# Kernel optimization log

Measured on AMD Instinct MI355X. Metric: run time of the kernel, lower is better.

The kernel has to match this reference:

```python
import jax, jax.numpy as jnp
import numpy as np
import math

FRAME_SIZE = 576
GAMMA = 0.5
NUM_HEADS = 32


def rotate_half(x):
    x1, x2 = jnp.split(x, 2, axis=-1)
    return jnp.concatenate([-x2, x1], axis=-1)


def apply_rope(x, freqs):
    return x * jnp.cos(freqs) + rotate_half(x) * jnp.sin(freqs)


def rope_freqs(length, dim):
    theta = 10000.0 ** (-jnp.arange(0, dim, 2, dtype=jnp.float32) / dim)
    f = jnp.arange(length, dtype=jnp.float32)[:, None] * theta[None, :]  # [L, dim/2]
    return jnp.concatenate([f, f], axis=-1)  # [L, dim]


def setup_inputs() -> dict:
    key = jax.random.key(0)
    ks = jax.random.split(key, 9)
    B, T, C = 2, 2048, 2048
    s = 0.02  # init scale for projection weights
    return {
        "hidden_states": jax.random.normal(ks[0], (B, T, C), jnp.float32),
        "Wq": jax.random.normal(ks[1], (C, C), jnp.float32) * s,
        "bq": jnp.zeros((C,), jnp.float32),
        "Wk": jax.random.normal(ks[2], (C, C), jnp.float32) * s,
        "bk": jnp.zeros((C,), jnp.float32),
        "Wv": jax.random.normal(ks[3], (C, C), jnp.float32) * s,
        "bv": jnp.zeros((C,), jnp.float32),
        "Wo": jax.random.normal(ks[4], (C, C), jnp.float32) * s,
        "bo": jnp.zeros((C,), jnp.float32),
    }


def reference(hidden_states, Wq, bq, Wk, bk, Wv, bv, Wo, bo):
    B, T, C = hidden_states.shape
    H = NUM_HEADS
    dh = C // H

    def split_heads(x):
        return x.reshape(B, T, H, dh).transpose(0, 2, 1, 3)  # [B,H,T,dh]

    q = split_heads(hidden_states @ Wq.T + bq)
    k = split_heads(hidden_states @ Wk.T + bk)
    v = split_heads(hidden_states @ Wv.T + bv)

    # Dual RoPE: absolute positions, then temporal (frame-level) positions.
    freqs_abs = rope_freqs(T, dh)[None, None]  # [1,1,T,dh]
    q = apply_rope(q, freqs_abs)
    k = apply_rope(k, freqs_abs)

    temporal_ids = jnp.floor((jnp.arange(T) // FRAME_SIZE).astype(jnp.float32) * GAMMA).astype(jnp.int32)
    n_temp = int(math.floor(((T - 1) // FRAME_SIZE) * GAMMA)) + 1
    freqs_temp = rope_freqs(n_temp, dh)[temporal_ids][None, None]  # [1,1,T,dh]
    q = apply_rope(q, freqs_temp)
    k = apply_rope(k, freqs_temp)

    scores = jnp.einsum('bhqd,bhkd->bhqk', q, k) / math.sqrt(dh)
    # build_fwbc_mask reduces to a plain causal mask (inner-loop var leak: j==i).
    causal = jnp.tril(jnp.ones((T, T), dtype=bool))
    scores = jnp.where(causal[None, None], scores, -jnp.inf)
    weights = jax.nn.softmax(scores, axis=-1)

    out = jnp.einsum('bhqk,bhkd->bhqd', weights, v)
    out = out.transpose(0, 2, 1, 3).reshape(B, T, H * dh)
    return out @ Wo.T + bo
```

## Files before the change

kernel.cpp:

```cpp
#include <hip/hip_runtime.h>
#include <hip/hip_bf16.h>

#define AS1 __attribute__((address_space(1)))
#define AS3 __attribute__((address_space(3)))

typedef __attribute__((ext_vector_type(8))) short bf16x8;
typedef __attribute__((ext_vector_type(4))) float f32x4;

__device__ __forceinline__ unsigned short f2bf(float f) {
    unsigned int u = __float_as_uint(f);
    u += 0x7fffu + ((u >> 16) & 1u);
    return (unsigned short)(u >> 16);
}

__device__ __forceinline__ unsigned int pk2bf(float a, float b) {
    __hip_bfloat162 h = __float22bfloat162_rn(make_float2(a, b));
    return *reinterpret_cast<unsigned int*>(&h);
}

__device__ __forceinline__ void gload16(const void* g, void* l) {
    __builtin_amdgcn_global_load_lds((const AS1 unsigned int*)g, (AS3 unsigned int*)l, 16, 0, 0);
}

#define MFMA(a, b, c) __builtin_amdgcn_mfma_f32_16x16x32_bf16(a, b, c, 0, 0, 0)

__global__ void cvt_f32_bf16(const float* __restrict__ src, unsigned short* __restrict__ dst, int n4) {
    const int i = blockIdx.x * blockDim.x + threadIdx.x;
    if (i >= n4) return;
    const float4 v = reinterpret_cast<const float4*>(src)[i];
    ushort4 o;
    o.x = f2bf(v.x); o.y = f2bf(v.y); o.z = f2bf(v.z); o.w = f2bf(v.w);
    reinterpret_cast<ushort4*>(dst)[i] = o;
}

__global__ void rope_table(float* __restrict__ cosT, float* __restrict__ sinT) {
    const int i = blockIdx.x * 256 + threadIdx.x;
    const int t = i >> 5, j = i & 31;
    const int fid = t / 576;
    const float p = (float)(t + (fid >> 1));
    const float theta = powf(10000.0f, -(float)j / 32.0f);
    const float ang = p * theta;
    cosT[i] = cosf(ang);
    sinT[i] = sinf(ang);
}

template <int MODE>
__global__ __launch_bounds__(256, 2)
void gemm128(const unsigned short* __restrict__ A,
             const unsigned short* __restrict__ W,
             const float* __restrict__ b0, const float* __restrict__ b1, const float* __restrict__ b2,
             const float* __restrict__ cosT, const float* __restrict__ sinT,
             unsigned short* __restrict__ O0, unsigned short* __restrict__ O1, unsigned short* __restrict__ O2,
             float* __restrict__ Of) {
    constexpr int K = 2048, LDA = 2048;
    const int tid = threadIdx.x;
    const int lane = tid & 63;
    const int w = tid >> 6;
    const int wr = w >> 1, wc = w & 1;
    const int brow = blockIdx.y * 128;
    const int bcol = blockIdx.x * 128;
    const int z = blockIdx.z;
    const unsigned short* Bmat = W + (size_t)z * 4194304;
    const float* bias = (MODE == 1) ? b0 : (z == 0 ? b0 : (z == 1 ? b1 : b2));

    __shared__ unsigned char lds[32768];
    unsigned char* Asm_ = lds;
    unsigned char* Bsm  = lds + 16384;

    f32x4 acc[4][4] = {};
    const int l15 = lane & 15;
    const int lg = lane >> 4;

    for (int kt = 0; kt < K / 64; ++kt) {
        const int k0g = kt * 64;
        __syncthreads();
#pragma unroll
        for (int s = 0; s < 4; ++s) {
            const int c = w * 256 + s * 64 + lane;
            const int row = c >> 3;
            const int cb = (c & 7) ^ (row & 7);
            gload16(A    + (size_t)(brow + row) * LDA + k0g + cb * 8, Asm_ + (w * 256 + s * 64) * 16);
            gload16(Bmat + (size_t)(bcol + row) * LDA + k0g + cb * 8, Bsm  + (w * 256 + s * 64) * 16);
        }
        asm volatile("s_waitcnt vmcnt(0)" ::: "memory");
        __syncthreads();

#pragma unroll
        for (int kk = 0; kk < 2; ++kk) {
            bf16x8 af[4], bfr[4];
            const int koff = kk * 64 + lg * 16;
#pragma unroll
            for (int m = 0; m < 4; ++m) {
                const int row = wr * 64 + m * 16 + l15;
                af[m] = *(const bf16x8*)(Asm_ + row * 128 + (koff ^ ((row & 7) << 4)));
            }
#pragma unroll
            for (int n = 0; n < 4; ++n) {
                const int row = wc * 64 + n * 16 + l15;
                bfr[n] = *(const bf16x8*)(Bsm + row * 128 + (koff ^ ((row & 7) << 4)));
            }
#pragma unroll
            for (int m = 0; m < 4; ++m)
#pragma unroll
                for (int n = 0; n < 4; ++n)
                    acc[m][n] = MFMA(af[m], bfr[n], acc[m][n]);
        }
    }

    if (MODE == 0 && z != 2) {
        const float qsc = (z == 0) ? 0.18033688011112042f : 1.0f;
        unsigned short* Ot = (z == 0 ? O0 : O1);
#pragma unroll
        for (int m = 0; m < 4; ++m) {
#pragma unroll
            for (int n2 = 0; n2 < 2; ++n2) {
                const int d1 = n2 * 16 + l15;
                const int cg1 = bcol + wc * 64 + d1;
                const float bv1 = bias[cg1], bv2 = bias[cg1 + 32];
                const int hh = cg1 >> 6;
#pragma unroll
                for (int r = 0; r < 4; ++r) {
                    const int rg = brow + wr * 64 + m * 16 + lg * 4 + r;
                    const int bb = rg >> 11, t = rg & 2047;
                    const float v1 = acc[m][n2][r] + bv1;
                    const float v2 = acc[m][n2 + 2][r] + bv2;
                    const float c = cosT[t * 32 + d1];
                    const float s = sinT[t * 32 + d1];
                    unsigned short* base = Ot + (((size_t)bb * 32 + hh) * 2048 + t) * 64;
                    base[d1]      = f2bf((v1 * c - v2 * s) * qsc);
                    base[d1 + 32] = f2bf((v2 * c + v1 * s) * qsc);
                }
            }
        }
    } else {
#pragma unroll
        for (int m = 0; m < 4; ++m) {
#pragma unroll
            for (int n = 0; n < 4; ++n) {
                const int cg = bcol + wc * 64 + n * 16 + l15;
                const float bv_ = bias[cg];
#pragma unroll
                for (int r = 0; r < 4; ++r) {
                    const int rg = brow + wr * 64 + m * 16 + lg * 4 + r;
                    const float v = acc[m][n][r] + bv_;
                    if (MODE == 0) {
                        const int bb = rg >> 11, t = rg & 2047, hh = cg >> 6, d = cg & 63;
                        O2[(((size_t)bb * 32 + hh) * 64 + d) * 2048 + t] = f2bf(v);
                    } else {
                        Of[(size_t)rg * 2048 + cg] = v;
                    }
                }
            }
        }
    }
}

__global__ __launch_bounds__(256, 4)
void attn(const unsigned short* __restrict__ Qg, const unsigned short* __restrict__ Kg,
          const unsigned short* __restrict__ Vtg, unsigned short* __restrict__ Og) {
    const int d0 = blockIdx.x;
    const int xcd = d0 & 7, ii = d0 >> 3;
    const int bh = xcd * 8 + (ii >> 4);
    const int pp = ii & 15;
    const int b = bh >> 5, h = bh & 31;
    const int tid = threadIdx.x;
    const int lane = tid & 63;
    const int w = tid >> 6;
    const int l15 = lane & 15, lg = lane >> 4;

    const unsigned short* Q  = Qg  + (size_t)bh * 131072;
    const unsigned short* K  = Kg  + (size_t)bh * 131072;
    const unsigned short* Vt = Vtg + (size_t)bh * 131072;

    __shared__ unsigned char Ks[2][8192];
    __shared__ unsigned char Vs[2][8192];
    __shared__ unsigned char Ps[4][2048];

    const int cA = (w << 6) + lane, cB = cA + 256;
    const int rA = cA >> 3, bA_ = (cA & 7) ^ (rA & 7);
    const int rB = cB >> 3, bB_ = (cB & 7) ^ (rB & 7);
    const int dstA = (w << 10);
    const int dstB = 4096 + (w << 10);

#define STAGE(kt_, buf_)                                                          \
    do {                                                                          \
        const int ko = (kt_) * 64;                                                \
        gload16(K  + (size_t)(ko + rA) * 64 + bA_ * 8, Ks[buf_] + dstA);          \
        gload16(K  + (size_t)(ko + rB) * 64 + bB_ * 8, Ks[buf_] + dstB);          \
        gload16(Vt + (size_t)rA * 2048 + ko + bA_ * 8, Vs[buf_] + dstA);          \
        gload16(Vt + (size_t)rB * 2048 + ko + bB_ * 8, Vs[buf_] + dstB);          \
    } while (0)

    const int pbase = l15 * 128;
    const int pswz = (l15 & 7) << 4;
    const int lg8 = lg * 8;

    for (int pass = 0; pass < 2; ++pass) {
        const int qt = pass ? (31 - pp) : pp;
        const int qbase = qt * 64 + w * 16;

        bf16x8 qf[2];
#pragma unroll
        for (int h2 = 0; h2 < 2; ++h2)
            qf[h2] = *(const bf16x8*)(Q + (size_t)(qbase + l15) * 64 + h2 * 32 + lg * 8);

        f32x4 oacc[4] = {};
        float m = -1e30f;
        float l = 0.f;

        __syncthreads();
        const int ntiles = qt + 1;
        STAGE(0, 0);

        for (int kt = 0; kt < ntiles; ++kt) {
            const int buf = kt & 1;
            asm volatile("s_waitcnt vmcnt(0)" ::: "memory");
            __syncthreads();
            if (kt + 1 < ntiles) STAGE(kt + 1, buf ^ 1);

            const bool diag = (kt == qt);
            const int ntmax = diag ? w : 3;

            f32x4 sac[4] = {};
            __builtin_amdgcn_s_setprio(1);
#pragma unroll
            for (int nt = 0; nt < 4; ++nt) {
                if (nt <= ntmax) {
#pragma unroll
                    for (int h2 = 0; h2 < 2; ++h2) {
                        const int kcol = nt * 16 + l15;
                        const int koff = h2 * 64 + lg * 16;
                        const bf16x8 kf = *(const bf16x8*)(Ks[buf] + kcol * 128 + (koff ^ ((kcol & 7) << 4)));
                        sac[nt] = MFMA(kf, qf[h2], sac[nt]);
                    }
                }
            }
            __builtin_amdgcn_s_setprio(0);

            if (diag) {
#pragma unroll
                for (int nt = 0; nt < 4; ++nt) {
                    if (nt == w) {
#pragma unroll
                        for (int r = 0; r < 4; ++r)
                            if (lg * 4 + r > l15) sac[nt][r] = -1e30f;
                    }
                }
            }

            float pm = -1e30f;
#pragma unroll
            for (int nt = 0; nt < 4; ++nt) {
                if (nt <= ntmax) {
#pragma unroll
                    for (int r = 0; r < 4; ++r) pm = fmaxf(pm, sac[nt][r]);
                }
            }
            pm = fmaxf(pm, __shfl_xor(pm, 16));
            pm = fmaxf(pm, __shfl_xor(pm, 32));

            if (!__all(pm - m <= 8.0f)) {
                const float mn = fmaxf(m, pm);
                const float sc = exp2f(m - mn);
                m = mn;
                l *= sc;
                float scp[4];
#pragma unroll
                for (int r = 0; r < 4; ++r) scp[r] = __shfl(sc, (lg << 2) + r);
#pragma unroll
                for (int dt = 0; dt < 4; ++dt)
#pragma unroll
                    for (int r = 0; r < 4; ++r) oacc[dt][r] *= scp[r];
            }

#pragma unroll
            for (int nt = 0; nt < 4; ++nt) {
                unsigned long long pk = 0;
                if (nt <= ntmax) {
                    const float p0 = exp2f(sac[nt][0] - m);
                    const float p1 = exp2f(sac[nt][1] - m);
                    const float p2 = exp2f(sac[nt][2] - m);
                    const float p3 = exp2f(sac[nt][3] - m);
                    l += (p0 + p1) + (p2 + p3);
                    pk = ((unsigned long long)pk2bf(p2, p3) << 32) | pk2bf(p0, p1);
                }
                *(unsigned long long*)(Ps[w] + pbase + ((nt * 32 + lg8) ^ pswz)) = pk;
            }

            asm volatile("s_waitcnt lgkmcnt(0)" ::: "memory");
            __builtin_amdgcn_sched_barrier(0);

            const int h2max = (ntmax >= 2) ? 1 : 0;
            __builtin_amdgcn_s_setprio(1);
#pragma unroll
            for (int h2 = 0; h2 < 2; ++h2) {
                if (h2 > h2max) continue;
                const int koff = h2 * 64 + lg * 16;
                const bf16x8 pf = *(const bf16x8*)(Ps[w] + pbase + (koff ^ pswz));
#pragma unroll
                for (int dt = 0; dt < 4; ++dt) {
                    const int dcol = dt * 16 + l15;
                    const bf16x8 vf = *(const bf16x8*)(Vs[buf] + dcol * 128 + (koff ^ ((dcol & 7) << 4)));
                    oacc[dt] = MFMA(pf, vf, oacc[dt]);
                }
            }
            __builtin_amdgcn_s_setprio(0);
        }

        float lf = l;
        lf += __shfl_xor(lf, 16);
        lf += __shfl_xor(lf, 32);
        float lq[4];
#pragma unroll
        for (int r = 0; r < 4; ++r) lq[r] = __shfl(lf, (lg << 2) + r);
#pragma unroll
        for (int dt = 0; dt < 4; ++dt) {
#pragma unroll
            for (int r = 0; r < 4; ++r) {
                const int t = qbase + lg * 4 + r;
                const float v = oacc[dt][r] / lq[r];
                Og[(size_t)(b * 2048 + t) * 2048 + h * 64 + dt * 16 + l15] = f2bf(v);
            }
        }
    }
#undef STAGE
}

extern "C" void kernel_launch(void* const* d_in, const int* in_sizes, int n_in,
                              void* d_out, int out_size, void* d_ws, size_t ws_size,
                              hipStream_t stream) {
    const float* hs = (const float*)d_in[0];
    const float* Wq = (const float*)d_in[1];
    const float* bq = (const float*)d_in[2];
    const float* Wk = (const float*)d_in[3];
    const float* bk = (const float*)d_in[4];
    const float* Wv = (const float*)d_in[5];
    const float* bv = (const float*)d_in[6];
    const float* Wo = (const float*)d_in[7];
    const float* bo = (const float*)d_in[8];
    float* out = (float*)d_out;

    char* ws = (char*)d_ws;
    unsigned short* Xb = (unsigned short*)ws;
    unsigned short* Wb = (unsigned short*)(ws + (16u << 20));
    unsigned short* Qb = (unsigned short*)(ws + (48u << 20));
    unsigned short* Kb = (unsigned short*)(ws + (64u << 20));
    unsigned short* Vtb = (unsigned short*)(ws + (80u << 20));
    unsigned short* Ob = Xb;
    float* cosT = (float*)(ws + (96u << 20));
    float* sinT = cosT + 65536;

    cvt_f32_bf16<<<8192, 256, 0, stream>>>(hs, Xb, 2097152);
    cvt_f32_bf16<<<4096, 256, 0, stream>>>(Wq, Wb + (size_t)0 * 4194304, 1048576);
    cvt_f32_bf16<<<4096, 256, 0, stream>>>(Wk, Wb + (size_t)1 * 4194304, 1048576);
    cvt_f32_bf16<<<4096, 256, 0, stream>>>(Wv, Wb + (size_t)2 * 4194304, 1048576);
    cvt_f32_bf16<<<4096, 256, 0, stream>>>(Wo, Wb + (size_t)3 * 4194304, 1048576);
    rope_table<<<256, 256, 0, stream>>>(cosT, sinT);

    gemm128<0><<<dim3(16, 32, 3), 256, 0, stream>>>(Xb, Wb, bq, bk, bv, cosT, sinT, Qb, Kb, Vtb, nullptr);

    attn<<<dim3(1024), 256, 0, stream>>>(Qb, Kb, Vtb, Ob);

    gemm128<1><<<dim3(16, 32, 1), 256, 0, stream>>>(Ob, Wb + (size_t)3 * 4194304, bo, bo, bo,
                                                    cosT, sinT, nullptr, nullptr, nullptr, out);
}
```

Before: 273.9 us.

## Rewrite projection GEMMs as 256x128 tiles with triple-buffered async LDS pipeline

Replaces the 128x128 single-buffered GEMM with a 512-thread 256x128 tile kernel that keeps three LDS stages in flight. Global-to-LDS loads for stage t+2 are interleaved with MFMA groups under barriers and raised wave priority. Workgroup IDs are remapped so tiles are grouped per XCD for L2 reuse. The QKV projection now runs as a flat 1D grid with the weight matrix selected from the column tile. The aim is to hide global-memory latency and cut load traffic per FLOP, at the cost of 144KB of LDS per block, which limits occupancy.

Measured after the change: 280.7 us. 1.02x slower.

```diff
diff --git a/kernel.cpp b/kernel.cpp
--- a/kernel.cpp
+++ b/kernel.cpp
@@ -45,111 +45,167 @@
 }
 
 template <int MODE>
-__global__ __launch_bounds__(256, 2)
-void gemm128(const unsigned short* __restrict__ A,
+__global__ __launch_bounds__(512, 2)
+void gemm256(const unsigned short* __restrict__ A,
              const unsigned short* __restrict__ W,
              const float* __restrict__ b0, const float* __restrict__ b1, const float* __restrict__ b2,
              const float* __restrict__ cosT, const float* __restrict__ sinT,
              unsigned short* __restrict__ O0, unsigned short* __restrict__ O1, unsigned short* __restrict__ O2,
              float* __restrict__ Of) {
-    constexpr int K = 2048, LDA = 2048;
+    constexpr int NT = 32;
+    const int nwg = (MODE == 0) ? 768 : 256;
+    const int cpx = nwg >> 3;
+    const int orig = blockIdx.x;
+    const int newid = (orig & 7) * cpx + (orig >> 3);
+    const int by = newid & 15;
+    const int bx = newid >> 4;
+
     const int tid = threadIdx.x;
     const int lane = tid & 63;
     const int w = tid >> 6;
-    const int wr = w >> 1, wc = w & 1;
-    const int brow = blockIdx.y * 128;
-    const int bcol = blockIdx.x * 128;
-    const int z = blockIdx.z;
-    const unsigned short* Bmat = W + (size_t)z * 4194304;
-    const float* bias = (MODE == 1) ? b0 : (z == 0 ? b0 : (z == 1 ? b1 : b2));
-
-    __shared__ unsigned char lds[32768];
-    unsigned char* Asm_ = lds;
-    unsigned char* Bsm  = lds + 16384;
-
-    f32x4 acc[4][4] = {};
-    const int l15 = lane & 15;
-    const int lg = lane >> 4;
-
-    for (int kt = 0; kt < K / 64; ++kt) {
-        const int k0g = kt * 64;
-        __syncthreads();
-#pragma unroll
-        for (int s = 0; s < 4; ++s) {
-            const int c = w * 256 + s * 64 + lane;
-            const int row = c >> 3;
-            const int cb = (c & 7) ^ (row & 7);
-            gload16(A    + (size_t)(brow + row) * LDA + k0g + cb * 8, Asm_ + (w * 256 + s * 64) * 16);
-            gload16(Bmat + (size_t)(bcol + row) * LDA + k0g + cb * 8, Bsm  + (w * 256 + s * 64) * 16);
-        }
-        asm volatile("s_waitcnt vmcnt(0)" ::: "memory");
-        __syncthreads();
-
-#pragma unroll
-        for (int kk = 0; kk < 2; ++kk) {
-            bf16x8 af[4], bfr[4];
-            const int koff = kk * 64 + lg * 16;
-#pragma unroll
-            for (int m = 0; m < 4; ++m) {
-                const int row = wr * 64 + m * 16 + l15;
-                af[m] = *(const bf16x8*)(Asm_ + row * 128 + (koff ^ ((row & 7) << 4)));
-            }
-#pragma unroll
-            for (int n = 0; n < 4; ++n) {
-                const int row = wc * 64 + n * 16 + l15;
-                bfr[n] = *(const bf16x8*)(Bsm + row * 128 + (koff ^ ((row & 7) << 4)));
-            }
-#pragma unroll
-            for (int m = 0; m < 4; ++m)
-#pragma unroll
-                for (int n = 0; n < 4; ++n)
-                    acc[m][n] = MFMA(af[m], bfr[n], acc[m][n]);
-        }
+    const int wr = w >> 2, wc = w & 3;
+    const int l15 = lane & 15, lg = lane >> 4;
+    const int brow = by * 256;
+    const int bcol = bx * 128;
+
+    __shared__ unsigned char lds[147456];
+
+    const int c0 = w * 128 + lane;
+    const int c1 = c0 + 64;
+    const int r0 = c0 >> 3, k0_ = ((c0 & 7) ^ (r0 & 7)) * 8;
+    const int r1 = c1 >> 3, k1_ = ((c1 & 7) ^ (r1 & 7)) * 8;
+    const int dA0 = w * 2048, dA1 = w * 2048 + 1024;
+
+#define STG_A(t_, h_, bp_) do {                                                            \
+        gload16(A + (size_t)(brow + (h_)*128 + r0) * 2048 + (t_)*64 + k0_, (bp_) + (h_)*16384 + dA0); \
+        gload16(A + (size_t)(brow + (h_)*128 + r1) * 2048 + (t_)*64 + k1_, (bp_) + (h_)*16384 + dA1); \
+    } while (0)
+#define STG_B(t_, bp_) do {                                                                \
+        gload16(W + (size_t)(bcol + r0) * 2048 + (t_)*64 + k0_, (bp_) + 32768 + dA0);      \
+        gload16(W + (size_t)(bcol + r1) * 2048 + (t_)*64 + k1_, (bp_) + 32768 + dA1);      \
+    } while (0)
+
+    f32x4 acc[8][2] = {};
+
+    const int aswz = (l15 & 7) << 4;
+    const int kof0 = (lg * 16) ^ aswz;
+    const int kof1 = (64 + lg * 16) ^ aswz;
+    const int abase = (wr * 128 + l15) * 128;
+    const int bbase = ((wc >> 1) * 64 + (wc & 1) * 16 + l15) * 128 + 32768;
+
+    {
+        unsigned char* p0 = lds;
+        unsigned char* p1 = lds + 49152;
+        STG_A(0, 0, p0); STG_A(0, 1, p0); STG_B(0, p0);
+        STG_A(1, 0, p1); STG_A(1, 1, p1); STG_B(1, p1);
     }
-
-    if (MODE == 0 && z != 2) {
-        const float qsc = (z == 0) ? 0.18033688011112042f : 1.0f;
-        unsigned short* Ot = (z == 0 ? O0 : O1);
-#pragma unroll
-        for (int m = 0; m < 4; ++m) {
-#pragma unroll
-            for (int n2 = 0; n2 < 2; ++n2) {
-                const int d1 = n2 * 16 + l15;
-                const int cg1 = bcol + wc * 64 + d1;
-                const float bv1 = bias[cg1], bv2 = bias[cg1 + 32];
-                const int hh = cg1 >> 6;
+    asm volatile("s_waitcnt vmcnt(6)" ::: "memory");
+    __syncthreads();
+
+#define MM(mi, m_) do {                                          \
+        acc[m_][0] = MFMA(af[mi][0], bfr[0][0], acc[m_][0]);     \
+        acc[m_][0] = MFMA(af[mi][1], bfr[0][1], acc[m_][0]);     \
+        acc[m_][1] = MFMA(af[mi][0], bfr[1][0], acc[m_][1]);     \
+        acc[m_][1] = MFMA(af[mi][1], bfr[1][1], acc[m_][1]);     \
+    } while (0)
+
+#define LDA_PAIR(p_) do {                                                         \
+        af[0][0] = *(const bf16x8*)(bt + abase + (2*(p_)) * 2048 + kof0);         \
+        af[0][1] = *(const bf16x8*)(bt + abase + (2*(p_)) * 2048 + kof1);         \
+        af[1][0] = *(const bf16x8*)(bt + abase + (2*(p_)+1) * 2048 + kof0);       \
+        af[1][1] = *(const bf16x8*)(bt + abase + (2*(p_)+1) * 2048 + kof1);       \
+    } while (0)
+
+#define DO_MFMA(p_) do {                                         \
+        __builtin_amdgcn_s_barrier();                            \
+        __builtin_amdgcn_s_setprio(1);                           \
+        MM(0, 2*(p_)); MM(1, 2*(p_)+1);                          \
+        __builtin_amdgcn_s_setprio(0);                           \
+        __builtin_amdgcn_s_barrier();                            \
+    } while (0)
+
+    for (int t = 0; t < NT; ++t) {
+        unsigned char* bt = lds + (t % 3) * 49152;
+        unsigned char* bs = lds + ((t + 2) % 3) * 49152;
+        const bool pre = (t + 2 < NT);
+        bf16x8 bfr[2][2], af[2][2];
+
+        bfr[0][0] = *(const bf16x8*)(bt + bbase + kof0);
+        bfr[0][1] = *(const bf16x8*)(bt + bbase + kof1);
+        bfr[1][0] = *(const bf16x8*)(bt + bbase + 4096 + kof0);
+        bfr[1][1] = *(const bf16x8*)(bt + bbase + 4096 + kof1);
+        LDA_PAIR(0);
+        if (pre) STG_A(t + 2, 0, bs);
+        DO_MFMA(0);
+
+        LDA_PAIR(1);
+        if (pre) STG_A(t + 2, 1, bs);
+        DO_MFMA(1);
+
+        LDA_PAIR(2);
+        if (pre) STG_B(t + 2, bs);
+        DO_MFMA(2);
+
+        LDA_PAIR(3);
+        if (pre) { asm volatile("s_waitcnt vmcnt(6)" ::: "memory"); }
+        else     { asm volatile("s_waitcnt vmcnt(0)" ::: "memory"); }
+        DO_MFMA(3);
+    }
+#undef STG_A
+#undef STG_B
+#undef MM
+#undef LDA_PAIR
+#undef DO_MFMA
+
+    if (MODE == 0) {
+        const int z = bx >> 4;
+        const int bxl = bx & 15;
+        const int hh = bxl * 2 + (wc >> 1);
+        const int d1 = (wc & 1) * 16 + l15;
+        const int cgz = hh * 64 + d1;
+        const float* bias = (z == 0) ? b0 : (z == 1 ? b1 : b2);
+        const float bv1 = bias[cgz], bv2 = bias[cgz + 32];
+        if (z < 2) {
+            const float qsc = (z == 0) ? 0.18033688011112042f : 1.0f;
+            unsigned short* Ot = (z == 0) ? O0 : O1;
+#pragma unroll
+            for (int m = 0; m < 8; ++m) {
 #pragma unroll
                 for (int r = 0; r < 4; ++r) {
-                    const int rg = brow + wr * 64 + m * 16 + lg * 4 + r;
-                    const int bb = rg >> 11, t = rg & 2047;
-                    const float v1 = acc[m][n2][r] + bv1;
-                    const float v2 = acc[m][n2 + 2][r] + bv2;
-                    const float c = cosT[t * 32 + d1];
-                    const float s = sinT[t * 32 + d1];
-                    unsigned short* base = Ot + (((size_t)bb * 32 + hh) * 2048 + t) * 64;
+                    const int rg = brow + wr * 128 + m * 16 + lg * 4 + r;
+                    const int bb = rg >> 11, tt = rg & 2047;
+                    const float v1 = acc[m][0][r] + bv1;
+                    const float v2 = acc[m][1][r] + bv2;
+                    const float c = cosT[tt * 32 + d1];
+                    const float s = sinT[tt * 32 + d1];
+                    unsigned short* base = Ot + (((size_t)bb * 32 + hh) * 2048 + tt) * 64;
                     base[d1]      = f2bf((v1 * c - v2 * s) * qsc);
                     base[d1 + 32] = f2bf((v2 * c + v1 * s) * qsc);
                 }
             }
+        } else {
+#pragma unroll
+            for (int m = 0; m < 8; ++m) {
+#pragma unroll
+                for (int r = 0; r < 4; ++r) {
+                    const int rg = brow + wr * 128 + m * 16 + lg * 4 + r;
+                    const int bb = rg >> 11, tt = rg & 2047;
+                    unsigned short* Vb = O2 + ((size_t)bb * 32 + hh) * 131072 + tt;
+                    Vb[(size_t)d1 * 2048]        = f2bf(acc[m][0][r] + bv1);
+                    Vb[(size_t)(d1 + 32) * 2048] = f2bf(acc[m][1][r] + bv2);
+                }
+            }
         }
     } else {
-#pragma unroll
-        for (int m = 0; m < 4; ++m) {
-#pragma unroll
-            for (int n = 0; n < 4; ++n) {
-                const int cg = bcol + wc * 64 + n * 16 + l15;
-                const float bv_ = bias[cg];
-#pragma unroll
-                for (int r = 0; r < 4; ++r) {
-                    const int rg = brow + wr * 64 + m * 16 + lg * 4 + r;
-                    const float v = acc[m][n][r] + bv_;
-                    if (MODE == 0) {
-                        const int bb = rg >> 11, t = rg & 2047, hh = cg >> 6, d = cg & 63;
-                        O2[(((size_t)bb * 32 + hh) * 64 + d) * 2048 + t] = f2bf(v);
-                    } else {
-                        Of[(size_t)rg * 2048 + cg] = v;
-                    }
-                }
+        const int cg = bcol + (wc >> 1) * 64 + (wc & 1) * 16 + l15;
+        const float bv1 = b0[cg], bv2 = b0[cg + 32];
+#pragma unroll
+        for (int m = 0; m < 8; ++m) {
+#pragma unroll
+            for (int r = 0; r < 4; ++r) {
+                const int rg = brow + wr * 128 + m * 16 + lg * 4 + r;
+                Of[(size_t)rg * 2048 + cg]      = acc[m][0][r] + bv1;
+                Of[(size_t)rg * 2048 + cg + 32] = acc[m][1][r] + bv2;
             }
         }
     }
@@ -357,10 +413,10 @@
     cvt_f32_bf16<<<4096, 256, 0, stream>>>(Wo, Wb + (size_t)3 * 4194304, 1048576);
     rope_table<<<256, 256, 0, stream>>>(cosT, sinT);
 
-    gemm128<0><<<dim3(16, 32, 3), 256, 0, stream>>>(Xb, Wb, bq, bk, bv, cosT, sinT, Qb, Kb, Vtb, nullptr);
+    gemm256<0><<<dim3(768), 512, 0, stream>>>(Xb, Wb, bq, bk, bv, cosT, sinT, Qb, Kb, Vtb, nullptr);
 
     attn<<<dim3(1024), 256, 0, stream>>>(Qb, Kb, Vtb, Ob);
 
-    gemm128<1><<<dim3(16, 32, 1), 256, 0, stream>>>(Ob, Wb + (size_t)3 * 4194304, bo, bo, bo,
-                                                    cosT, sinT, nullptr, nullptr, nullptr, out);
-}
+    gemm256<1><<<dim3(256), 512, 0, stream>>>(Ob, Wb + (size_t)3 * 4194304, bo, bo, bo,
+                                              cosT, sinT, nullptr, nullptr, nullptr, out);
+}
```

## Replace QKV projection with 256x256-tile double-buffered pipelined GEMM kernel

Applied to the files above, without the earlier changes.

Adds a dedicated QKV GEMM kernel that uses 256x256 output tiles with 512 threads and 128KB of LDS. It double-buffers async global-to-LDS loads interleaved with MFMA phases, using setprio and barriers, and remaps block IDs for XCD locality. The concatenated Q/K/V weights are treated as one N=6144 matrix, with the RoPE epilogue kept. The aim is more data reuse per tile and overlap of memory loads with compute, in place of the old load-wait-compute loop. The costs are heavy LDS and register use and a fragile hand-scheduled waitcnt sequence.

New measurement: 284.1 us. 3.7% more time.

```diff
diff --git a/kernel.cpp b/kernel.cpp
--- a/kernel.cpp
+++ b/kernel.cpp
@@ -44,13 +44,179 @@
     sinT[i] = sinf(ang);
 }
 
+__global__ __launch_bounds__(512, 2)
+void gemmqkv(const unsigned short* __restrict__ A,
+             const unsigned short* __restrict__ W,
+             const float* __restrict__ b0, const float* __restrict__ b1, const float* __restrict__ b2,
+             const float* __restrict__ cosT, const float* __restrict__ sinT,
+             unsigned short* __restrict__ O0, unsigned short* __restrict__ O1,
+             unsigned short* __restrict__ O2) {
+    const int orig = blockIdx.x;
+    const int newid = (orig & 7) * 48 + (orig >> 3);
+    const int by = newid / 24, bx = newid % 24;
+    const int brow = by * 256;
+    const int bcol = bx * 256;
+
+    const int tid = threadIdx.x;
+    const int lane = tid & 63;
+    const int w = tid >> 6;
+    const int wr = w >> 2, wc = w & 3;
+    const int l15 = lane & 15, lg = lane >> 4;
+
+    __shared__ unsigned char lds[131072];
+
+    const int r0 = tid >> 2;
+    const int q0 = (tid & 3) ^ ((r0 + (r0 >> 2)) & 3);
+    const int r1 = r0 + 128;
+    const int q1 = (tid & 3) ^ ((r1 + (r1 >> 2)) & 3);
+    const unsigned short* pA0 = A + (size_t)(brow + r0) * 2048 + q0 * 8;
+    const unsigned short* pA1 = A + (size_t)(brow + r1) * 2048 + q1 * 8;
+    const unsigned short* pB0 = W + (size_t)(bcol + r0) * 2048 + q0 * 8;
+    const unsigned short* pB1 = W + (size_t)(bcol + r1) * 2048 + q1 * 8;
+    const int dst0 = w * 1024, dst1 = 8192 + w * 1024;
+
+#define AB_(buf, kh) (lds + (buf) * 32768 + (kh) * 16384)
+#define BB_(buf, kh) (lds + 65536 + (buf) * 32768 + (kh) * 16384)
+#define STG_A(t_, kh, buf) do { \
+        gload16(pA0 + (t_) * 64 + (kh) * 32, AB_(buf, kh) + dst0); \
+        gload16(pA1 + (t_) * 64 + (kh) * 32, AB_(buf, kh) + dst1); } while (0)
+#define STG_B(t_, kh, buf) do { \
+        gload16(pB0 + (t_) * 64 + (kh) * 32, BB_(buf, kh) + dst0); \
+        gload16(pB1 + (t_) * 64 + (kh) * 32, BB_(buf, kh) + dst1); } while (0)
+
+    int aoff[8], boff[4];
+#pragma unroll
+    for (int m = 0; m < 8; ++m) {
+        const int r = wr * 128 + m * 16 + l15;
+        aoff[m] = (r * 4 + (lg ^ ((r + (r >> 2)) & 3))) * 16;
+    }
+#pragma unroll
+    for (int n = 0; n < 4; ++n) {
+        const int r = wc * 64 + n * 16 + l15;
+        boff[n] = (r * 4 + (lg ^ ((r + (r >> 2)) & 3))) * 16;
+    }
+
+    f32x4 acc[8][4] = {};
+    bf16x8 af[4], bf[4];
+
+    STG_A(0, 0, 0); STG_B(0, 0, 0); STG_A(0, 1, 0); STG_B(0, 1, 0);
+    STG_A(1, 0, 1); STG_B(1, 0, 1);
+    asm volatile("s_waitcnt vmcnt(4)" ::: "memory");
+    __builtin_amdgcn_s_barrier();
+
+#define LDA4(g, kh, buf) do { \
+        af[0] = *(const bf16x8*)(AB_(buf, kh) + aoff[(g) * 4 + 0]); \
+        af[1] = *(const bf16x8*)(AB_(buf, kh) + aoff[(g) * 4 + 1]); \
+        af[2] = *(const bf16x8*)(AB_(buf, kh) + aoff[(g) * 4 + 2]); \
+        af[3] = *(const bf16x8*)(AB_(buf, kh) + aoff[(g) * 4 + 3]); } while (0)
+#define LDB4(kh, buf) do { \
+        bf[0] = *(const bf16x8*)(BB_(buf, kh) + boff[0]); \
+        bf[1] = *(const bf16x8*)(BB_(buf, kh) + boff[1]); \
+        bf[2] = *(const bf16x8*)(BB_(buf, kh) + boff[2]); \
+        bf[3] = *(const bf16x8*)(BB_(buf, kh) + boff[3]); } while (0)
+#define MM16(g) do { \
+        __builtin_amdgcn_s_setprio(1); \
+        _Pragma("unroll") for (int mm = 0; mm < 4; ++mm) \
+        _Pragma("unroll") for (int n = 0; n < 4; ++n) \
+            acc[(g) * 4 + mm][n] = MFMA(af[mm], bf[n], acc[(g) * 4 + mm][n]); \
+        __builtin_amdgcn_s_setprio(0); } while (0)
+#define LGKM0 do { asm volatile("s_waitcnt lgkmcnt(0)" ::: "memory"); \
+                   __builtin_amdgcn_sched_barrier(0); } while (0)
+#define BAR __builtin_amdgcn_s_barrier()
+
+    for (int j = 0; j < 16; ++j) {
+        const int u = 2 * j;
+        const bool pre = (j < 15);
+        LDA4(0, 0, 0); LDB4(0, 0);
+        STG_A(u + 1, 1, 1);
+        BAR; LGKM0; MM16(0); BAR;
+        LDA4(1, 0, 0);
+        STG_B(u + 1, 1, 1);
+        BAR; LGKM0; MM16(1); BAR;
+        LDA4(0, 1, 0); LDB4(1, 0);
+        if (pre) STG_A(u + 2, 0, 0);
+        BAR; LGKM0; MM16(0); BAR;
+        LDA4(1, 1, 0);
+        if (pre) STG_B(u + 2, 0, 0);
+        BAR; LGKM0; MM16(1);
+        if (pre) { asm volatile("s_waitcnt vmcnt(4)" ::: "memory"); }
+        else     { asm volatile("s_waitcnt vmcnt(0)" ::: "memory"); }
+        BAR;
+        LDA4(0, 0, 1); LDB4(0, 1);
+        if (pre) STG_A(u + 2, 1, 0);
+        BAR; LGKM0; MM16(0); BAR;
+        LDA4(1, 0, 1);
+        if (pre) STG_B(u + 2, 1, 0);
+        BAR; LGKM0; MM16(1); BAR;
+        LDA4(0, 1, 1); LDB4(1, 1);
+        if (pre) STG_A(u + 3, 0, 1);
+        BAR; LGKM0; MM16(0); BAR;
+        LDA4(1, 1, 1);
+        if (pre) STG_B(u + 3, 0, 1);
+        BAR; LGKM0; MM16(1);
+        if (pre) { asm volatile("s_waitcnt vmcnt(4)" ::: "memory"); }
+        else     { asm volatile("s_waitcnt vmcnt(0)" ::: "memory"); }
+        BAR;
+    }
+#undef STG_A
+#undef STG_B
+#undef AB_
+#undef BB_
+#undef LDA4
+#undef LDB4
+#undef MM16
+#undef LGKM0
+#undef BAR
+
+    const int z = bx >> 3;
+    const int hh = (bx & 7) * 4 + wc;
+    const float* bias = (z == 0) ? b0 : (z == 1 ? b1 : b2);
+    if (z < 2) {
+        const float qsc = (z == 0) ? 0.18033688011112042f : 1.0f;
+        unsigned short* Ot = (z == 0) ? O0 : O1;
+#pragma unroll
+        for (int n2 = 0; n2 < 2; ++n2) {
+            const int d1 = n2 * 16 + l15;
+            const float bv1 = bias[hh * 64 + d1], bv2 = bias[hh * 64 + d1 + 32];
+#pragma unroll
+            for (int m = 0; m < 8; ++m) {
+#pragma unroll
+                for (int r = 0; r < 4; ++r) {
+                    const int rg = brow + wr * 128 + m * 16 + lg * 4 + r;
+                    const int bb = rg >> 11, tt = rg & 2047;
+                    const float v1 = acc[m][n2][r] + bv1;
+                    const float v2 = acc[m][n2 + 2][r] + bv2;
+                    const float c = cosT[tt * 32 + d1];
+                    const float s = sinT[tt * 32 + d1];
+                    unsigned short* base = Ot + (((size_t)bb * 32 + hh) * 2048 + tt) * 64;
+                    base[d1]      = f2bf((v1 * c - v2 * s) * qsc);
+                    base[d1 + 32] = f2bf((v2 * c + v1 * s) * qsc);
+                }
+            }
+        }
+    } else {
+#pragma unroll
+        for (int n = 0; n < 4; ++n) {
+            const int d = n * 16 + l15;
+            const float bv_ = bias[hh * 64 + d];
+#pragma unroll
+            for (int m = 0; m < 8; ++m) {
+#pragma unroll
+                for (int r = 0; r < 4; ++r) {
+                    const int rg = brow + wr * 128 + m * 16 + lg * 4 + r;
+                    const int bb = rg >> 11, tt = rg & 2047;
+                    O2[(((size_t)bb * 32 + hh) * 64 + d) * 2048 + tt] = f2bf(acc[m][n][r] + bv_);
+                }
+            }
+        }
+    }
+}
+
 template <int MODE>
 __global__ __launch_bounds__(256, 2)
 void gemm128(const unsigned short* __restrict__ A,
              const unsigned short* __restrict__ W,
-             const float* __restrict__ b0, const float* __restrict__ b1, const float* __restrict__ b2,
-             const float* __restrict__ cosT, const float* __restrict__ sinT,
-             unsigned short* __restrict__ O0, unsigned short* __restrict__ O1, unsigned short* __restrict__ O2,
+             const float* __restrict__ b0,
              float* __restrict__ Of) {
     constexpr int K = 2048, LDA = 2048;
     const int tid = threadIdx.x;
@@ -59,9 +225,6 @@
     const int wr = w >> 1, wc = w & 1;
     const int brow = blockIdx.y * 128;
     const int bcol = blockIdx.x * 128;
-    const int z = blockIdx.z;
-    const unsigned short* Bmat = W + (size_t)z * 4194304;
-    const float* bias = (MODE == 1) ? b0 : (z == 0 ? b0 : (z == 1 ? b1 : b2));
 
     __shared__ unsigned char lds[32768];
     unsigned char* Asm_ = lds;
@@ -79,8 +242,8 @@
             const int c = w * 256 + s * 64 + lane;
             const int row = c >> 3;
             const int cb = (c & 7) ^ (row & 7);
-            gload16(A    + (size_t)(brow + row) * LDA + k0g + cb * 8, Asm_ + (w * 256 + s * 64) * 16);
-            gload16(Bmat + (size_t)(bcol + row) * LDA + k0g + cb * 8, Bsm  + (w * 256 + s * 64) * 16);
+            gload16(A + (size_t)(brow + row) * LDA + k0g + cb * 8, Asm_ + (w * 256 + s * 64) * 16);
+            gload16(W + (size_t)(bcol + row) * LDA + k0g + cb * 8, Bsm  + (w * 256 + s * 64) * 16);
         }
         asm volatile("s_waitcnt vmcnt(0)" ::: "memory");
         __syncthreads();
@@ -107,49 +270,16 @@
         }
     }
 
-    if (MODE == 0 && z != 2) {
-        const float qsc = (z == 0) ? 0.18033688011112042f : 1.0f;
-        unsigned short* Ot = (z == 0 ? O0 : O1);
-#pragma unroll
-        for (int m = 0; m < 4; ++m) {
-#pragma unroll
-            for (int n2 = 0; n2 < 2; ++n2) {
-                const int d1 = n2 * 16 + l15;
-                const int cg1 = bcol + wc * 64 + d1;
-                const float bv1 = bias[cg1], bv2 = bias[cg1 + 32];
-                const int hh = cg1 >> 6;
-#pragma unroll
-                for (int r = 0; r < 4; ++r) {
-                    const int rg = brow + wr * 64 + m * 16 + lg * 4 + r;
-                    const int bb = rg >> 11, t = rg & 2047;
-                    const float v1 = acc[m][n2][r] + bv1;
-                    const float v2 = acc[m][n2 + 2][r] + bv2;
-                    const float c = cosT[t * 32 + d1];
-                    const float s = sinT[t * 32 + d1];
-                    unsigned short* base = Ot + (((size_t)bb * 32 + hh) * 2048 + t) * 64;
-                    base[d1]      = f2bf((v1 * c - v2 * s) * qsc);
-                    base[d1 + 32] = f2bf((v2 * c + v1 * s) * qsc);
-                }
-            }
-        }
-    } else {
-#pragma unroll
-        for (int m = 0; m < 4; ++m) {
-#pragma unroll
-            for (int n = 0; n < 4; ++n) {
-                const int cg = bcol + wc * 64 + n * 16 + l15;
-                const float bv_ = bias[cg];
-#pragma unroll
-                for (int r = 0; r < 4; ++r) {
-                    const int rg = brow + wr * 64 + m * 16 + lg * 4 + r;
-                    const float v = acc[m][n][r] + bv_;
-                    if (MODE == 0) {
-                        const int bb = rg >> 11, t = rg & 2047, hh = cg >> 6, d = cg & 63;
-                        O2[(((size_t)bb * 32 + hh) * 64 + d) * 2048 + t] = f2bf(v);
-                    } else {
-                        Of[(size_t)rg * 2048 + cg] = v;
-                    }
-                }
+#pragma unroll
+    for (int m = 0; m < 4; ++m) {
+#pragma unroll
+        for (int n = 0; n < 4; ++n) {
+            const int cg = bcol + wc * 64 + n * 16 + l15;
+            const float bv_ = b0[cg];
+#pragma unroll
+            for (int r = 0; r < 4; ++r) {
+                const int rg = brow + wr * 64 + m * 16 + lg * 4 + r;
+                Of[(size_t)rg * 2048 + cg] = acc[m][n][r] + bv_;
             }
         }
     }
@@ -357,10 +487,9 @@
     cvt_f32_bf16<<<4096, 256, 0, stream>>>(Wo, Wb + (size_t)3 * 4194304, 1048576);
     rope_table<<<256, 256, 0, stream>>>(cosT, sinT);
 
-    gemm128<0><<<dim3(16, 32, 3), 256, 0, stream>>>(Xb, Wb, bq, bk, bv, cosT, sinT, Qb, Kb, Vtb, nullptr);
+    gemmqkv<<<dim3(384), 512, 0, stream>>>(Xb, Wb, bq, bk, bv, cosT, sinT, Qb, Kb, Vtb);
 
     attn<<<dim3(1024), 256, 0, stream>>>(Qb, Kb, Vtb, Ob);
 
-    gemm128<1><<<dim3(16, 32, 1), 256, 0, stream>>>(Ob, Wb + (size_t)3 * 4194304, bo, bo, bo,
-                                                    cosT, sinT, nullptr, nullptr, nullptr, out);
-}
+    gemm128<1><<<dim3(16, 32, 1), 256, 0, stream>>>(Ob, Wb + (size_t)3 * 4194304, bo, out);
+}
```

## Process 128-row query tiles per attention block and merge weight conversions

Applied to the files above, without the earlier changes.

The attention kernel now gives each warp two 16-row query sub-tiles, so every block covers 128 queries. Each K/V tile staged in LDS is reused for twice as many MFMAs, and the grid is halved to 512 blocks. Causal skipping and masking are recomputed per sub-tile, and launch bounds drop to 2 waves per SIMD to fit the doubled accumulators. The four weight conversion launches are merged into one 2D-grid kernel to cut launch overhead. The cost is higher register pressure, lower occupancy and fewer blocks to balance across CUs.

Measured after the change: 289.8 us. +5.8%, slower.

```diff
diff --git a/kernel.cpp b/kernel.cpp
--- a/kernel.cpp
+++ b/kernel.cpp
@@ -31,6 +31,18 @@
     ushort4 o;
     o.x = f2bf(v.x); o.y = f2bf(v.y); o.z = f2bf(v.z); o.w = f2bf(v.w);
     reinterpret_cast<ushort4*>(dst)[i] = o;
+}
+
+__global__ void cvt_w4(const float* __restrict__ Wq, const float* __restrict__ Wk,
+                       const float* __restrict__ Wv, const float* __restrict__ Wo,
+                       unsigned short* __restrict__ dst) {
+    const int z = blockIdx.y;
+    const float* src = (z == 0) ? Wq : (z == 1) ? Wk : (z == 2) ? Wv : Wo;
+    const int i = blockIdx.x * 256 + threadIdx.x;
+    const float4 v = reinterpret_cast<const float4*>(src)[i];
+    ushort4 o;
+    o.x = f2bf(v.x); o.y = f2bf(v.y); o.z = f2bf(v.z); o.w = f2bf(v.w);
+    reinterpret_cast<ushort4*>(dst + (size_t)z * 4194304)[i] = o;
 }
 
 __global__ void rope_table(float* __restrict__ cosT, float* __restrict__ sinT) {
@@ -155,13 +167,13 @@
     }
 }
 
-__global__ __launch_bounds__(256, 4)
+__global__ __launch_bounds__(256, 2)
 void attn(const unsigned short* __restrict__ Qg, const unsigned short* __restrict__ Kg,
           const unsigned short* __restrict__ Vtg, unsigned short* __restrict__ Og) {
     const int d0 = blockIdx.x;
     const int xcd = d0 & 7, ii = d0 >> 3;
-    const int bh = xcd * 8 + (ii >> 4);
-    const int pp = ii & 15;
+    const int bh = xcd * 8 + (ii >> 3);
+    const int pp = ii & 7;
     const int b = bh >> 5, h = bh & 31;
     const int tid = threadIdx.x;
     const int lane = tid & 63;
@@ -174,7 +186,7 @@
 
     __shared__ unsigned char Ks[2][8192];
     __shared__ unsigned char Vs[2][8192];
-    __shared__ unsigned char Ps[4][2048];
+    __shared__ unsigned char Ps[4][2][2048];
 
     const int cA = (w << 6) + lane, cB = cA + 256;
     const int rA = cA >> 3, bA_ = (cA & 7) ^ (rA & 7);
@@ -196,20 +208,21 @@
     const int lg8 = lg * 8;
 
     for (int pass = 0; pass < 2; ++pass) {
-        const int qt = pass ? (31 - pp) : pp;
-        const int qbase = qt * 64 + w * 16;
-
-        bf16x8 qf[2];
-#pragma unroll
-        for (int h2 = 0; h2 < 2; ++h2)
-            qf[h2] = *(const bf16x8*)(Q + (size_t)(qbase + l15) * 64 + h2 * 32 + lg * 8);
-
-        f32x4 oacc[4] = {};
-        float m = -1e30f;
-        float l = 0.f;
+        const int qt = pass ? (15 - pp) : pp;
+
+        bf16x8 qf[2][2];
+#pragma unroll
+        for (int m = 0; m < 2; ++m)
+#pragma unroll
+            for (int h2 = 0; h2 < 2; ++h2)
+                qf[m][h2] = *(const bf16x8*)(Q + (size_t)(qt * 128 + w * 32 + m * 16 + l15) * 64 + h2 * 32 + lg * 8);
+
+        f32x4 oacc0[4] = {}, oacc1[4] = {};
+        float m0 = -1e30f, m1 = -1e30f;
+        float l0 = 0.f, l1 = 0.f;
 
         __syncthreads();
-        const int ntiles = qt + 1;
+        const int ntiles = 2 * qt + 2;
         STAGE(0, 0);
 
         for (int kt = 0; kt < ntiles; ++kt) {
@@ -218,108 +231,155 @@
             __syncthreads();
             if (kt + 1 < ntiles) STAGE(kt + 1, buf ^ 1);
 
-            const bool diag = (kt == qt);
-            const int ntmax = diag ? w : 3;
-
-            f32x4 sac[4] = {};
+            const int koff_t = kt * 64 - qt * 128;
+            const int vs0 = w * 32 - koff_t;
+            const int vs1 = vs0 + 16;
+            const bool do0 = (vs0 >= 0);
+            const bool do1 = (vs1 >= 0);
+            const int ntm0 = (vs0 >> 4) > 3 ? 3 : (vs0 >> 4);
+            const int ntm1 = (vs1 >> 4) > 3 ? 3 : (vs1 >> 4);
+
+            if (!do1) continue;
+
+            f32x4 sac0[4] = {}, sac1[4] = {};
             __builtin_amdgcn_s_setprio(1);
 #pragma unroll
             for (int nt = 0; nt < 4; ++nt) {
-                if (nt <= ntmax) {
+                if (nt <= ntm1) {
 #pragma unroll
                     for (int h2 = 0; h2 < 2; ++h2) {
                         const int kcol = nt * 16 + l15;
                         const int koff = h2 * 64 + lg * 16;
                         const bf16x8 kf = *(const bf16x8*)(Ks[buf] + kcol * 128 + (koff ^ ((kcol & 7) << 4)));
-                        sac[nt] = MFMA(kf, qf[h2], sac[nt]);
+                        sac1[nt] = MFMA(kf, qf[1][h2], sac1[nt]);
+                        if (do0 && nt <= ntm0) sac0[nt] = MFMA(kf, qf[0][h2], sac0[nt]);
                     }
                 }
             }
             __builtin_amdgcn_s_setprio(0);
 
-            if (diag) {
-#pragma unroll
-                for (int nt = 0; nt < 4; ++nt) {
-                    if (nt == w) {
-#pragma unroll
-                        for (int r = 0; r < 4; ++r)
-                            if (lg * 4 + r > l15) sac[nt][r] = -1e30f;
+            const int dnt0 = vs0 >> 4, dnt1 = vs1 >> 4;
+#pragma unroll
+            for (int nt = 0; nt < 4; ++nt) {
+                if (nt == dnt1) {
+#pragma unroll
+                    for (int r = 0; r < 4; ++r)
+                        if (lg * 4 + r > l15) sac1[nt][r] = -1e30f;
+                }
+                if (do0 && nt == dnt0) {
+#pragma unroll
+                    for (int r = 0; r < 4; ++r)
+                        if (lg * 4 + r > l15) sac0[nt][r] = -1e30f;
+                }
+            }
+
+            float pm0 = -1e30f, pm1 = -1e30f;
+#pragma unroll
+            for (int nt = 0; nt < 4; ++nt) {
+                if (nt <= ntm1) {
+#pragma unroll
+                    for (int r = 0; r < 4; ++r) pm1 = fmaxf(pm1, sac1[nt][r]);
+                }
+                if (do0 && nt <= ntm0) {
+#pragma unroll
+                    for (int r = 0; r < 4; ++r) pm0 = fmaxf(pm0, sac0[nt][r]);
+                }
+            }
+            pm1 = fmaxf(pm1, __shfl_xor(pm1, 16));
+            pm1 = fmaxf(pm1, __shfl_xor(pm1, 32));
+            if (do0) {
+                pm0 = fmaxf(pm0, __shfl_xor(pm0, 16));
+                pm0 = fmaxf(pm0, __shfl_xor(pm0, 32));
+            }
+
+            if (!__all(fmaxf(pm0 - m0, pm1 - m1) <= 8.0f)) {
+                const float mn0 = fmaxf(m0, pm0), mn1 = fmaxf(m1, pm1);
+                const float sc0 = exp2f(m0 - mn0), sc1 = exp2f(m1 - mn1);
+                m0 = mn0; m1 = mn1;
+                l0 *= sc0; l1 *= sc1;
+                float s0p[4], s1p[4];
+#pragma unroll
+                for (int r = 0; r < 4; ++r) {
+                    s0p[r] = __shfl(sc0, (lg << 2) + r);
+                    s1p[r] = __shfl(sc1, (lg << 2) + r);
+                }
+#pragma unroll
+                for (int dt = 0; dt < 4; ++dt)
+#pragma unroll
+                    for (int r = 0; r < 4; ++r) {
+                        oacc0[dt][r] *= s0p[r];
+                        oacc1[dt][r] *= s1p[r];
                     }
-                }
-            }
-
-            float pm = -1e30f;
-#pragma unroll
-            for (int nt = 0; nt < 4; ++nt) {
-                if (nt <= ntmax) {
-#pragma unroll
-                    for (int r = 0; r < 4; ++r) pm = fmaxf(pm, sac[nt][r]);
-                }
-            }
-            pm = fmaxf(pm, __shfl_xor(pm, 16));
-            pm = fmaxf(pm, __shfl_xor(pm, 32));
-
-            if (!__all(pm - m <= 8.0f)) {
-                const float mn = fmaxf(m, pm);
-                const float sc = exp2f(m - mn);
-                m = mn;
-                l *= sc;
-                float scp[4];
-#pragma unroll
-                for (int r = 0; r < 4; ++r) scp[r] = __shfl(sc, (lg << 2) + r);
-#pragma unroll
-                for (int dt = 0; dt < 4; ++dt)
-#pragma unroll
-                    for (int r = 0; r < 4; ++r) oacc[dt][r] *= scp[r];
             }
 
 #pragma unroll
             for (int nt = 0; nt < 4; ++nt) {
                 unsigned long long pk = 0;
-                if (nt <= ntmax) {
-                    const float p0 = exp2f(sac[nt][0] - m);
-                    const float p1 = exp2f(sac[nt][1] - m);
-                    const float p2 = exp2f(sac[nt][2] - m);
-                    const float p3 = exp2f(sac[nt][3] - m);
-                    l += (p0 + p1) + (p2 + p3);
+                if (nt <= ntm1) {
+                    const float p0 = exp2f(sac1[nt][0] - m1);
+                    const float p1 = exp2f(sac1[nt][1] - m1);
+                    const float p2 = exp2f(sac1[nt][2] - m1);
+                    const float p3 = exp2f(sac1[nt][3] - m1);
+                    l1 += (p0 + p1) + (p2 + p3);
                     pk = ((unsigned long long)pk2bf(p2, p3) << 32) | pk2bf(p0, p1);
                 }
-                *(unsigned long long*)(Ps[w] + pbase + ((nt * 32 + lg8) ^ pswz)) = pk;
+                *(unsigned long long*)(Ps[w][1] + pbase + ((nt * 32 + lg8) ^ pswz)) = pk;
+                if (do0) {
+                    unsigned long long qk = 0;
+                    if (nt <= ntm0) {
+                        const float p0 = exp2f(sac0[nt][0] - m0);
+                        const float p1 = exp2f(sac0[nt][1] - m0);
+                        const float p2 = exp2f(sac0[nt][2] - m0);
+                        const float p3 = exp2f(sac0[nt][3] - m0);
+                        l0 += (p0 + p1) + (p2 + p3);
+                        qk = ((unsigned long long)pk2bf(p2, p3) << 32) | pk2bf(p0, p1);
+                    }
+                    *(unsigned long long*)(Ps[w][0] + pbase + ((nt * 32 + lg8) ^ pswz)) = qk;
+                }
             }
 
             asm volatile("s_waitcnt lgkmcnt(0)" ::: "memory");
             __builtin_amdgcn_sched_barrier(0);
 
-            const int h2max = (ntmax >= 2) ? 1 : 0;
+            const int h2m0 = do0 ? ((ntm0 >= 2) ? 1 : 0) : -1;
+            const int h2m1 = (ntm1 >= 2) ? 1 : 0;
             __builtin_amdgcn_s_setprio(1);
 #pragma unroll
             for (int h2 = 0; h2 < 2; ++h2) {
-                if (h2 > h2max) continue;
+                if (h2 > h2m1) continue;
                 const int koff = h2 * 64 + lg * 16;
-                const bf16x8 pf = *(const bf16x8*)(Ps[w] + pbase + (koff ^ pswz));
+                const bf16x8 pf1 = *(const bf16x8*)(Ps[w][1] + pbase + (koff ^ pswz));
+                bf16x8 pf0 = pf1;
+                const bool u0 = (h2 <= h2m0);
+                if (u0) pf0 = *(const bf16x8*)(Ps[w][0] + pbase + (koff ^ pswz));
 #pragma unroll
                 for (int dt = 0; dt < 4; ++dt) {
                     const int dcol = dt * 16 + l15;
                     const bf16x8 vf = *(const bf16x8*)(Vs[buf] + dcol * 128 + (koff ^ ((dcol & 7) << 4)));
-                    oacc[dt] = MFMA(pf, vf, oacc[dt]);
+                    oacc1[dt] = MFMA(pf1, vf, oacc1[dt]);
+                    if (u0) oacc0[dt] = MFMA(pf0, vf, oacc0[dt]);
                 }
             }
             __builtin_amdgcn_s_setprio(0);
         }
 
-        float lf = l;
-        lf += __shfl_xor(lf, 16);
-        lf += __shfl_xor(lf, 32);
-        float lq[4];
-#pragma unroll
-        for (int r = 0; r < 4; ++r) lq[r] = __shfl(lf, (lg << 2) + r);
-#pragma unroll
-        for (int dt = 0; dt < 4; ++dt) {
-#pragma unroll
-            for (int r = 0; r < 4; ++r) {
-                const int t = qbase + lg * 4 + r;
-                const float v = oacc[dt][r] / lq[r];
-                Og[(size_t)(b * 2048 + t) * 2048 + h * 64 + dt * 16 + l15] = f2bf(v);
+#pragma unroll
+        for (int m = 0; m < 2; ++m) {
+            float lf = m ? l1 : l0;
+            lf += __shfl_xor(lf, 16);
+            lf += __shfl_xor(lf, 32);
+            float lq[4];
+#pragma unroll
+            for (int r = 0; r < 4; ++r) lq[r] = __shfl(lf, (lg << 2) + r);
+            const int qb = qt * 128 + w * 32 + m * 16;
+#pragma unroll
+            for (int dt = 0; dt < 4; ++dt) {
+#pragma unroll
+                for (int r = 0; r < 4; ++r) {
+                    const int t = qb + lg * 4 + r;
+                    const float v = (m ? oacc1[dt][r] : oacc0[dt][r]) / lq[r];
+                    Og[(size_t)(b * 2048 + t) * 2048 + h * 64 + dt * 16 + l15] = f2bf(v);
+                }
             }
         }
     }
@@ -351,15 +411,12 @@
     float* sinT = cosT + 65536;
 
     cvt_f32_bf16<<<8192, 256, 0, stream>>>(hs, Xb, 2097152);
-    cvt_f32_bf16<<<4096, 256, 0, stream>>>(Wq, Wb + (size_t)0 * 4194304, 1048576);
-    cvt_f32_bf16<<<4096, 256, 0, stream>>>(Wk, Wb + (size_t)1 * 4194304, 1048576);
-    cvt_f32_bf16<<<4096, 256, 0, stream>>>(Wv, Wb + (size_t)2 * 4194304, 1048576);
-    cvt_f32_bf16<<<4096, 256, 0, stream>>>(Wo, Wb + (size_t)3 * 4194304, 1048576);
+    cvt_w4<<<dim3(4096, 4), 256, 0, stream>>>(Wq, Wk, Wv, Wo, Wb);
     rope_table<<<256, 256, 0, stream>>>(cosT, sinT);
 
     gemm128<0><<<dim3(16, 32, 3), 256, 0, stream>>>(Xb, Wb, bq, bk, bv, cosT, sinT, Qb, Kb, Vtb, nullptr);
 
-    attn<<<dim3(1024), 256, 0, stream>>>(Qb, Kb, Vtb, Ob);
+    attn<<<dim3(512), 256, 0, stream>>>(Qb, Kb, Vtb, Ob);
 
     gemm128<1><<<dim3(16, 32, 1), 256, 0, stream>>>(Ob, Wb + (size_t)3 * 4194304, bo, bo, bo,
                                                     cosT, sinT, nullptr, nullptr, nullptr, out);
```
